# Performance work log

Hardware: AMD Instinct MI355X
Metric: run time of the kernel (lower is better)

Reference implementation:

```python
import jax, jax.numpy as jnp
import numpy as np
import math

FEAT, HID, EMB, NCLS = 128, 128, 64, 10
N, E = 50000, 1600000
RATIO = 0.8


def graph_conv(x, src, dst, valid, w_rel, b_rel, w_root):
    # PyG GraphConv: out = lin_rel(sum_{j->i} x_j) + lin_root(x_i)
    msg = jnp.where(valid[:, None], x[src], 0.0)  # [E, C]
    seg = jnp.where(valid, dst, x.shape[0])       # invalid -> dummy bucket
    agg = jax.ops.segment_sum(msg, seg, num_segments=x.shape[0] + 1)[:-1]
    return agg @ w_rel.T + b_rel + x @ w_root.T


def topk_pool(x, src, dst, valid, weight):
    # PyG TopKPooling: score = tanh((x . w) / ||w||); keep top ceil(ratio*N)
    score = jnp.tanh((x @ weight) / jnp.linalg.norm(weight))
    k = int(math.ceil(RATIO * x.shape[0]))
    _, perm = jax.lax.top_k(score, k)
    xp = x[perm] * score[perm][:, None]
    mapping = jnp.full((x.shape[0],), -1, dtype=src.dtype)
    mapping = mapping.at[perm].set(jnp.arange(k, dtype=src.dtype))
    nsrc, ndst = mapping[src], mapping[dst]
    nvalid = valid & (nsrc >= 0) & (ndst >= 0)
    return xp, nsrc, ndst, nvalid, perm


def setup_inputs() -> dict:
    key = jax.random.key(0)
    ks = jax.random.split(key, 24)
    s = 0.05
    inp = {
        'x': jax.random.normal(ks[0], (N, FEAT), dtype=jnp.float32),
        'edge_index': jax.random.randint(ks[1], (2, E), 0, N, dtype=jnp.int32),
        'w1_rel': jax.random.normal(ks[2], (HID, FEAT)) * s,
        'w1_root': jax.random.normal(ks[3], (HID, FEAT)) * s,
        'b1': jnp.zeros((HID,), jnp.float32),
        'p1_w': jax.random.normal(ks[4], (HID,)) * s,
        'w2_rel': jax.random.normal(ks[5], (EMB, HID)) * s,
        'w2_root': jax.random.normal(ks[6], (EMB, HID)) * s,
        'b2': jnp.zeros((EMB,), jnp.float32),
        'p2_w': jax.random.normal(ks[7], (EMB,)) * s,
        'w3_rel': jax.random.normal(ks[8], (EMB, EMB)) * s,
        'w3_root': jax.random.normal(ks[9], (EMB, EMB)) * s,
        'b3': jnp.zeros((EMB,), jnp.float32),
        'w4_rel': jax.random.normal(ks[10], (HID, EMB)) * s,
        'w4_root': jax.random.normal(ks[11], (HID, EMB)) * s,
        'b4': jnp.zeros((HID,), jnp.float32),
        'w5_rel': jax.random.normal(ks[12], (FEAT, HID)) * s,
        'w5_root': jax.random.normal(ks[13], (FEAT, HID)) * s,
        'b5': jnp.zeros((FEAT,), jnp.float32),
        'lin_w': jax.random.normal(ks[14], (NCLS, FEAT)) * s,
        'lin_b': jnp.zeros((NCLS,), jnp.float32),
    }
    return inp


def reference(x, edge_index, w1_rel, w1_root, b1, p1_w, w2_rel, w2_root, b2, p2_w,
              w3_rel, w3_root, b3, w4_rel, w4_root, b4, w5_rel, w5_root, b5,
              lin_w, lin_b):
    src0, dst0 = edge_index[0], edge_index[1]
    valid0 = jnp.ones((src0.shape[0],), dtype=bool)

    x1 = jax.nn.relu(graph_conv(x, src0, dst0, valid0, w1_rel, b1, w1_root))
    xp1, src1, dst1, valid1, perm1 = topk_pool(x1, src0, dst0, valid0, p1_w)
    x2 = jax.nn.relu(graph_conv(xp1, src1, dst1, valid1, w2_rel, b2, w2_root))
    xp2, src2, dst2, valid2, perm2 = topk_pool(x2, src1, dst1, valid1, p2_w)
    x3 = jax.nn.relu(graph_conv(xp2, src2, dst2, valid2, w3_rel, b3, w3_root))
    # Unpool1: scatter x3 into zeros shaped like x2, then skip-add
    u1 = jnp.zeros((x2.shape[0], x3.shape[1]), x3.dtype).at[perm2].set(x3) + x2
    x4 = jax.nn.relu(graph_conv(u1, src1, dst1, valid1, w4_rel, b4, w4_root))
    # Unpool2
    u2 = jnp.zeros((x1.shape[0], x4.shape[1]), x4.dtype).at[perm1].set(x4) + x1
    x5 = jax.nn.relu(graph_conv(u2, src0, dst0, valid0, w5_rel, b5, w5_root))
    return jax.nn.log_softmax(x5 @ lin_w.T + lin_b, axis=-1)
```

## Files before the change

### kernel.cpp

```cpp
#include <hip/hip_runtime.h>
#include <hip/hip_bf16.h>
#include <math.h>

#define N0 50000
#define E0 1600000
#define K1 40000
#define K2 32000
#define FEAT 128
#define HID 128
#define EMB 64
#define NCLS 10

#define RADIX_BINS 4096

#define NB 391
#define PB_CH 8192
#define BCAP 5120

#define SCHUNK 2048

typedef __bf16 v8bf __attribute__((ext_vector_type(8)));
typedef __bf16 v4bf __attribute__((ext_vector_type(4)));
typedef float  v4f  __attribute__((ext_vector_type(4)));
typedef unsigned short u16;

static __device__ __forceinline__ unsigned f2key(float f) {
    unsigned u = __float_as_uint(f);
    return (u & 0x80000000u) ? ~u : (u | 0x80000000u);
}

__global__ void detect_dtype_kernel(const unsigned* __restrict__ w, int n, int* __restrict__ flag) {
    __shared__ int tot;
    if (threadIdx.x == 0) tot = 0;
    __syncthreads();
    int cnt = 0;
    for (int i = threadIdx.x; i < n; i += 256) {
        unsigned lo = w[i] & 0xFFFFu;
        unsigned e = (lo >> 7) & 0xFFu;
        cnt += (e >= 143);
    }
    atomicAdd(&tot, cnt);
    __syncthreads();
    if (threadIdx.x == 0) flag[0] = (tot > n / 8) ? 1 : 0;
}

static __device__ __forceinline__ float load_as_f32(const void* in, long long i, int isF32) {
    if (isF32) return ((const float*)in)[i];
    unsigned short h = ((const unsigned short*)in)[i];
    return __uint_as_float(((unsigned)h) << 16);
}

__global__ void x_convert_kernel(const void* __restrict__ in, float* __restrict__ xf,
                                 __bf16* __restrict__ hi, __bf16* __restrict__ lo, int n,
                                 const int* __restrict__ flag) {
    int i = blockIdx.x * 256 + threadIdx.x;
    if (i >= n) return;
    float v = load_as_f32(in, i, *flag);
    __bf16 h = (__bf16)v;
    int row = i >> 7, c = i & 127;
    xf[(((size_t)(c >> 4)) * N0 + row) * 16 + (c & 15)] = v;
    hi[i] = h; lo[i] = (__bf16)(v - (float)h);
}

struct SplitJob { const void* src; __bf16* hi; __bf16* lo; int n; };
struct SplitJobs { SplitJob j[10]; };
__global__ void split_all_kernel(SplitJobs jobs, const int* __restrict__ flag) {
    SplitJob jb = jobs.j[blockIdx.y];
    int i = blockIdx.x * 256 + threadIdx.x;
    if (i >= jb.n) return;
    float v = load_as_f32(jb.src, i, *flag);
    __bf16 h = (__bf16)v;
    jb.hi[i] = h; jb.lo[i] = (__bf16)(v - (float)h);
}

struct F32Job { const void* src; float* dst; int n; };
struct F32Jobs { F32Job j[9]; };
__global__ void f32_all_kernel(F32Jobs jobs, const int* __restrict__ flag) {
    F32Job jb = jobs.j[blockIdx.x];
    for (int i = threadIdx.x; i < jb.n; i += 256) jb.dst[i] = load_as_f32(jb.src, i, *flag);
}

__global__ void scan_reduce_kernel(const int* __restrict__ deg, int M, int* __restrict__ btot) {
    int t = threadIdx.x;
    int idx = blockIdx.x * SCHUNK + t * 8;
    int s = 0;
    if (idx + 8 <= M) {
        int4 a = *(const int4*)(deg + idx);
        int4 b = *(const int4*)(deg + idx + 4);
        s = a.x + a.y + a.z + a.w + b.x + b.y + b.z + b.w;
    } else {
        for (int k = 0; k < 8; ++k) if (idx + k < M) s += deg[idx + k];
    }
    for (int off = 32; off >= 1; off >>= 1) s += __shfl_xor(s, off, 64);
    __shared__ int ws[4];
    if ((t & 63) == 0) ws[t >> 6] = s;
    __syncthreads();
    if (t == 0) btot[blockIdx.x] = ws[0] + ws[1] + ws[2] + ws[3];
}

__global__ void scan_offsets_kernel(const int* __restrict__ btot, int nb,
                                    int* __restrict__ boff, int* __restrict__ totPtr) {
    int t = threadIdx.x;
    int v = (t < nb) ? btot[t] : 0;
    int incl = v;
    for (int off = 1; off < 64; off <<= 1) {
        int u = __shfl_up(incl, off, 64);
        if (t >= off) incl += u;
    }
    if (t < nb) boff[t] = incl - v;
    if (t == 63 && totPtr) totPtr[0] = incl;
}

__global__ void scan_apply_kernel(const int* __restrict__ deg, int M, const int* __restrict__ boff,
                                  int* __restrict__ rowptr) {
    int t = threadIdx.x;
    int lane = t & 63, wave = t >> 6;
    int idx = blockIdx.x * SCHUNK + t * 8;
    int v[8];
#pragma unroll
    for (int k = 0; k < 8; ++k) v[k] = (idx + k < M) ? deg[idx + k] : 0;
    int s = 0;
#pragma unroll
    for (int k = 0; k < 8; ++k) { int tmp = v[k]; v[k] = s; s += tmp; }
    int incl = s;
    for (int off = 1; off < 64; off <<= 1) {
        int u = __shfl_up(incl, off, 64);
        if (lane >= off) incl += u;
    }
    int texcl = incl - s;
    __shared__ int ws[4];
    if (lane == 63) ws[wave] = incl;
    __syncthreads();
    int woff = 0;
    for (int w = 0; w < 4; ++w) if (w < wave) woff += ws[w];
    int off0 = boff[blockIdx.x] + woff + texcl;
#pragma unroll
    for (int k = 0; k < 8; ++k) {
        int j = idx + k;
        if (j < M) rowptr[j] = off0 + v[k];
    }
}

struct SelCtl { unsigned long long prefix; int kRem; int counter; };

__global__ void scan_reduce_keys_kernel(const unsigned long long* __restrict__ keys, int M,
                                        const SelCtl* __restrict__ ctl, int* __restrict__ btot) {
    unsigned long long thr = ctl->prefix;
    int t = threadIdx.x;
    int idx = blockIdx.x * SCHUNK + t * 8;
    int s = 0;
#pragma unroll
    for (int k = 0; k < 8; ++k) if (idx + k < M) s += (keys[idx + k] >= thr);
    for (int off = 32; off >= 1; off >>= 1) s += __shfl_xor(s, off, 64);
    __shared__ int ws[4];
    if ((t & 63) == 0) ws[t >> 6] = s;
    __syncthreads();
    if (t == 0) btot[blockIdx.x] = ws[0] + ws[1] + ws[2] + ws[3];
}

__global__ void scan_apply_keys_kernel(const unsigned long long* __restrict__ keys, int M,
                                       const SelCtl* __restrict__ ctl, const int* __restrict__ boff,
                                       int* __restrict__ pos) {
    unsigned long long thr = ctl->prefix;
    int t = threadIdx.x;
    int lane = t & 63, wave = t >> 6;
    int idx = blockIdx.x * SCHUNK + t * 8;
    int v[8];
#pragma unroll
    for (int k = 0; k < 8; ++k) v[k] = (idx + k < M) ? (int)(keys[idx + k] >= thr) : 0;
    int s = 0;
#pragma unroll
    for (int k = 0; k < 8; ++k) { int tmp = v[k]; v[k] = s; s += tmp; }
    int incl = s;
    for (int off = 1; off < 64; off <<= 1) {
        int u = __shfl_up(incl, off, 64);
        if (lane >= off) incl += u;
    }
    int texcl = incl - s;
    __shared__ int ws[4];
    if (lane == 63) ws[wave] = incl;
    __syncthreads();
    int woff = 0;
    for (int w = 0; w < 4; ++w) if (w < wave) woff += ws[w];
    int off0 = boff[blockIdx.x] + woff + texcl;
#pragma unroll
    for (int k = 0; k < 8; ++k) {
        int j = idx + k;
        if (j < M) pos[j] = off0 + v[k];
    }
}

__global__ void bucket_count_kernel(const int* __restrict__ dst, int E, int* __restrict__ bktCnt) {
    __shared__ int cnt[NB];
    for (int b = threadIdx.x; b < NB; b += 256) cnt[b] = 0;
    __syncthreads();
    int e = blockIdx.x * PB_CH;
    int e1 = E < e + PB_CH ? E : e + PB_CH;
    for (int i = e + threadIdx.x; i < e1; i += 256)
        atomicAdd(&cnt[dst[i] >> 7], 1);
    __syncthreads();
    for (int b = threadIdx.x; b < NB; b += 256) {
        int c = cnt[b];
        if (c) atomicAdd(&bktCnt[b], c);
    }
}

__global__ void scan_nb_kernel(const int* __restrict__ bktCnt, int* __restrict__ bktBase,
                               int* __restrict__ bcur, int* __restrict__ rpM, int E) {
    __shared__ int sc[512];
    int t = threadIdx.x;
    int v = (t < NB) ? bktCnt[t] : 0;
    sc[t] = v;
    __syncthreads();
    for (int off = 1; off < 512; off <<= 1) {
        int u = 0;
        if (t >= off) u = sc[t - off];
        __syncthreads();
        if (t >= off) sc[t] += u;
        __syncthreads();
    }
    if (t < NB) {
        int base = sc[t] - v;
        bktBase[t] = base;
        bcur[t] = base;
    }
    if (t == 0) { bktBase[NB] = E; rpM[0] = E; }
}

__global__ void edge_partition_kernel(const int* __restrict__ src, const int* __restrict__ dst, int E,
                                      int* __restrict__ bcur, unsigned* __restrict__ pairBuf) {
    __shared__ int cnt[NB];
    __shared__ int bas[NB];
    for (int b = threadIdx.x; b < NB; b += 256) cnt[b] = 0;
    __syncthreads();
    int e0 = blockIdx.x * PB_CH;
    int e1 = E < e0 + PB_CH ? E : e0 + PB_CH;
    for (int e = e0 + threadIdx.x; e < e1; e += 256)
        atomicAdd(&cnt[dst[e] >> 7], 1);
    __syncthreads();
    for (int b = threadIdx.x; b < NB; b += 256) {
        int c = cnt[b];
        bas[b] = c ? atomicAdd(&bcur[b], c) : 0;
        cnt[b] = 0;
    }
    __syncthreads();
    for (int e = e0 + threadIdx.x; e < e1; e += 256) {
        int s = src[e];
        int d = dst[e];
        int b = d >> 7;
        int r = atomicAdd(&cnt[b], 1);
        unsigned pv = ((unsigned)(d & 127) << 16) | (unsigned)s;
        __builtin_nontemporal_store(pv, pairBuf + bas[b] + r);
    }
}

__global__ void bucket_fill_kernel(const unsigned* __restrict__ pairBuf, const int* __restrict__ bktBase,
                                   int Mrows, u16* __restrict__ cols, int* __restrict__ rowptr) {
    int b = blockIdx.x;
    int d0 = b << 7;
    int d1 = d0 + 128; if (d1 > Mrows) d1 = Mrows;
    int segBase = bktBase[b], segEnd = bktBase[b + 1];
    int size = segEnd - segBase;
    int tid = threadIdx.x;
    __shared__ int cnt[128];
    __shared__ int sc[128];
    __shared__ int cur[128];
    __shared__ u16 stage[BCAP];
    if (tid < 128) cnt[tid] = 0;
    __syncthreads();
    for (int t = tid; t < size; t += 256)
        atomicAdd(&cnt[pairBuf[segBase + t] >> 16], 1);
    __syncthreads();
    if (tid < 128) sc[tid] = cnt[tid];
    __syncthreads();
    for (int off = 1; off < 128; off <<= 1) {
        int u = 0;
        if (tid < 128 && tid >= off) u = sc[tid - off];
        __syncthreads();
        if (tid < 128 && tid >= off) sc[tid] += u;
        __syncthreads();
    }
    if (tid < 128) {
        int excl = sc[tid] - cnt[tid];
        cur[tid] = excl;
        if (d0 + tid < d1) rowptr[d0 + tid] = segBase + excl;
    }
    __syncthreads();
    if (size <= BCAP) {
        for (int t = tid; t < size; t += 256) {
            unsigned p = pairBuf[segBase + t];
            int pos = atomicAdd(&cur[p >> 16], 1);
            stage[pos] = (u16)(p & 0xFFFFu);
        }
        __syncthreads();
        for (int t = tid; t < size; t += 256)
            __builtin_nontemporal_store(stage[t], cols + segBase + t);
    } else {
        for (int t = tid; t < size; t += 256) {
            unsigned p = pairBuf[segBase + t];
            int pos = atomicAdd(&cur[p >> 16], 1);
            cols[segBase + pos] = (u16)(p & 0xFFFFu);
        }
    }
}

__global__ void deg_filter_kernel(const int* __restrict__ rowptr, const u16* __restrict__ cols,
                                  const int* __restrict__ map, int Mold, int* __restrict__ deg) {
    int d = blockIdx.x * 256 + threadIdx.x;
    if (d >= Mold) return;
    int nd = map[d];
    if (nd < 0) return;
    int b = rowptr[d], e = rowptr[d + 1];
    int c = 0;
    for (int j = b; j < e; ++j) c += (map[cols[j]] >= 0);
    deg[nd] = c;
}

__global__ void csr_filter_fill_kernel(const int* __restrict__ rowptr, const u16* __restrict__ cols,
                                       const int* __restrict__ map, int Mold,
                                       const int* __restrict__ newrp, u16* __restrict__ ncols) {
    int d = blockIdx.x * 256 + threadIdx.x;
    if (d >= Mold) return;
    int nd = map[d];
    if (nd < 0) return;
    int w = newrp[nd];
    int b = rowptr[d], e = rowptr[d + 1];
    for (int j = b; j < e; ++j) {
        int ns = map[cols[j]];
        if (ns >= 0) ncols[w++] = (u16)ns;
    }
}

template<int C>
__global__ void __launch_bounds__(256, 8)
aggregate_kernel(const int* __restrict__ rowptr, const u16* __restrict__ cols,
                 const float* __restrict__ xs, __bf16* __restrict__ aggHi,
                 __bf16* __restrict__ aggLo, int M) {
    const int SW = C / 8;
    const int LPR = SW / 4;
    const int RPB = 256 / LPR;
    int sl = blockIdx.x & 7;
    int n  = (blockIdx.x >> 3) * RPB + threadIdx.x / LPR;
    int c4 = threadIdx.x % LPR;
    if (n >= M) return;
    const float* xsl = xs + (size_t)sl * M * SW + (size_t)c4 * 4;
    int b = rowptr[n], e = rowptr[n + 1];
    float4 s = {0.f, 0.f, 0.f, 0.f};
    int j = b;
    for (; j + 8 <= e; j += 8) {
        int i0 = cols[j],     i1 = cols[j + 1], i2 = cols[j + 2], i3 = cols[j + 3];
        int i4 = cols[j + 4], i5 = cols[j + 5], i6 = cols[j + 6], i7 = cols[j + 7];
        float4 v0 = *(const float4*)(xsl + (size_t)i0 * SW);
        float4 v1 = *(const float4*)(xsl + (size_t)i1 * SW);
        float4 v2 = *(const float4*)(xsl + (size_t)i2 * SW);
        float4 v3 = *(const float4*)(xsl + (size_t)i3 * SW);
        float4 v4 = *(const float4*)(xsl + (size_t)i4 * SW);
        float4 v5 = *(const float4*)(xsl + (size_t)i5 * SW);
        float4 v6 = *(const float4*)(xsl + (size_t)i6 * SW);
        float4 v7 = *(const float4*)(xsl + (size_t)i7 * SW);
        s.x += v0.x; s.y += v0.y; s.z += v0.z; s.w += v0.w;
        s.x += v1.x; s.y += v1.y; s.z += v1.z; s.w += v1.w;
        s.x += v2.x; s.y += v2.y; s.z += v2.z; s.w += v2.w;
        s.x += v3.x; s.y += v3.y; s.z += v3.z; s.w += v3.w;
        s.x += v4.x; s.y += v4.y; s.z += v4.z; s.w += v4.w;
        s.x += v5.x; s.y += v5.y; s.z += v5.z; s.w += v5.w;
        s.x += v6.x; s.y += v6.y; s.z += v6.z; s.w += v6.w;
        s.x += v7.x; s.y += v7.y; s.z += v7.z; s.w += v7.w;
    }
    for (; j < e; ++j) {
        int i0 = cols[j];
        float4 v0 = *(const float4*)(xsl + (size_t)i0 * SW);
        s.x += v0.x; s.y += v0.y; s.z += v0.z; s.w += v0.w;
    }
    v4bf h, l;
    h[0] = (__bf16)s.x; l[0] = (__bf16)(s.x - (float)h[0]);
    h[1] = (__bf16)s.y; l[1] = (__bf16)(s.y - (float)h[1]);
    h[2] = (__bf16)s.z; l[2] = (__bf16)(s.z - (float)h[2]);
    h[3] = (__bf16)s.w; l[3] = (__bf16)(s.w - (float)h[3]);
    size_t o = ((size_t)sl * M + n) * SW + c4 * 4;
    __builtin_nontemporal_store(h, (v4bf*)(aggHi + o));
    __builtin_nontemporal_store(l, (v4bf*)(aggLo + o));
}

template<int Cin, int Cout>
__global__ void linear_mfma_kernel(int M,
                                   const __bf16* __restrict__ Ahi, const __bf16* __restrict__ Alo,
                                   const __bf16* __restrict__ WaHi, const __bf16* __restrict__ WaLo,
                                   const __bf16* __restrict__ Bhi, const __bf16* __restrict__ Blo,
                                   const __bf16* __restrict__ WbHi, const __bf16* __restrict__ WbLo,
                                   const float* __restrict__ bias, float* __restrict__ outF) {
    constexpr int NG = Cout / 16;
    constexpr int SW = Cin / 8;
    int wave = threadIdx.x >> 6;
    int lane = threadIdx.x & 63;
    int m = lane & 15, quad = lane >> 4;
    int row0 = blockIdx.x * 64 + wave * 16;
    int ra = row0 + m; if (ra > M - 1) ra = M - 1;

    v4f acc[NG];
#pragma unroll
    for (int g = 0; g < NG; ++g) acc[g] = (v4f){0.f, 0.f, 0.f, 0.f};

#pragma unroll
    for (int ks = 0; ks < Cin / 32; ++ks) {
        int col0 = ks * 32 + quad * 8;
        int sl = col0 / SW, off = col0 % SW;
        size_t aoff = ((size_t)sl * M + ra) * SW + off;
        v8bf ah = *(const v8bf*)(Ahi + aoff);
        v8bf al = *(const v8bf*)(Alo + aoff);
#pragma unroll
        for (int g = 0; g < NG; ++g) {
            size_t woff = (size_t)(g * 16 + m) * Cin + ks * 32 + quad * 8;
            v8bf bh = *(const v8bf*)(WaHi + woff);
            v8bf bl = *(const v8bf*)(WaLo + woff);
            acc[g] = __builtin_amdgcn_mfma_f32_16x16x32_bf16(ah, bh, acc[g], 0, 0, 0);
            acc[g] = __builtin_amdgcn_mfma_f32_16x16x32_bf16(ah, bl, acc[g], 0, 0, 0);
            acc[g] = __builtin_amdgcn_mfma_f32_16x16x32_bf16(al, bh, acc[g], 0, 0, 0);
        }
    }
#pragma unroll
    for (int ks = 0; ks < Cin / 32; ++ks) {
        size_t aoff = (size_t)ra * Cin + ks * 32 + quad * 8;
        v8bf ah = *(const v8bf*)(Bhi + aoff);
        v8bf al = *(const v8bf*)(Blo + aoff);
#pragma unroll
        for (int g = 0; g < NG; ++g) {
            size_t woff = (size_t)(g * 16 + m) * Cin + ks * 32 + quad * 8;
            v8bf bh = *(const v8bf*)(WbHi + woff);
            v8bf bl = *(const v8bf*)(WbLo + woff);
            acc[g] = __builtin_amdgcn_mfma_f32_16x16x32_bf16(ah, bh, acc[g], 0, 0, 0);
            acc[g] = __builtin_amdgcn_mfma_f32_16x16x32_bf16(ah, bl, acc[g], 0, 0, 0);
            acc[g] = __builtin_amdgcn_mfma_f32_16x16x32_bf16(al, bh, acc[g], 0, 0, 0);
        }
    }

#pragma unroll
    for (int g = 0; g < NG; ++g) {
        int col = g * 16 + m;
        float bv = bias[col];
#pragma unroll
        for (int r = 0; r < 4; ++r) {
            int row = row0 + quad * 4 + r;
            if (row < M) outF[(size_t)row * Cout + col] = fmaxf(acc[g][r] + bv, 0.f);
        }
    }
}

template<int C>
__global__ void score_kernel(const float* __restrict__ xin, const float* __restrict__ w,
                             int M, float* __restrict__ score, unsigned long long* __restrict__ keys) {
    int row = blockIdx.x * 4 + (threadIdx.x >> 6);
    int lane = threadIdx.x & 63;
    if (row >= M) return;
    float p = 0.f, q = 0.f;
#pragma unroll
    for (int c = lane; c < C; c += 64) {
        float wc = w[c];
        float xc = xin[(size_t)row * C + c];
        p += xc * wc; q += wc * wc;
    }
#pragma unroll
    for (int off = 32; off >= 1; off >>= 1) {
        p += __shfl_xor(p, off, 64);
        q += __shfl_xor(q, off, 64);
    }
    if (lane == 0) {
        float arg = p / sqrtf(q);
        float sc = (float)tanh((double)arg);
        score[row] = sc;
        keys[row] = ((unsigned long long)f2key(sc) << 16) |
                    (unsigned long long)(0xFFFFu ^ (unsigned)row);
    }
}

__global__ void radix_hist_kernel(const unsigned long long* __restrict__ keys, int N,
                                  int* __restrict__ hist, const SelCtl* __restrict__ ctl, int pass) {
    __shared__ int lh[RADIX_BINS];
    for (int b = threadIdx.x; b < RADIX_BINS; b += 256) lh[b] = 0;
    __syncthreads();
    int shift = 36 - 12 * pass;
    unsigned long long pref = (pass > 0) ? ctl->prefix : 0ull;
    for (int i = blockIdx.x * 256 + threadIdx.x; i < N; i += gridDim.x * 256) {
        unsigned long long key = keys[i];
        if (pass > 0 && (key >> (shift + 12)) != pref) continue;
        atomicAdd(&lh[(int)((key >> shift) & 0xFFFull)], 1);
    }
    __syncthreads();
    for (int b = threadIdx.x; b < RADIX_BINS; b += 256) {
        int c = lh[b];
        if (c) atomicAdd(&hist[b], c);
    }
}

__global__ void radix_select_kernel(int* __restrict__ hist, SelCtl* __restrict__ ctl,
                                    int K, int pass) {
    __shared__ int wtot[16];
    int t = threadIdx.x;
    int lane = t & 63, wave = t >> 6;
    int kRem = (pass == 0) ? K : ctl->kRem;
    unsigned long long oldPrefix = (pass == 0) ? 0ull : ctl->prefix;
    int base = t * 4;
    int h0 = hist[base], h1 = hist[base + 1], h2 = hist[base + 2], h3 = hist[base + 3];
    int tot = h0 + h1 + h2 + h3;
    int incl = tot;
#pragma unroll
    for (int off = 1; off < 64; off <<= 1) {
        int u = __shfl_down(incl, off, 64);
        if (lane + off < 64) incl += u;
    }
    if (lane == 0) wtot[wave] = incl;
    __syncthreads();
    int wsuf = 0;
#pragma unroll
    for (int w = 0; w < 16; ++w) if (w > wave) wsuf += wtot[w];
    int sExcl = wsuf + (incl - tot);
    if (sExcl < kRem && kRem <= sExcl + tot) {
        int c = sExcl;
        int hv[4] = {h0, h1, h2, h3};
        for (int k = 3; k >= 0; --k) {
            int h = hv[k];
            if (c + h >= kRem) {
                ctl->prefix = (oldPrefix << 12) | (unsigned long long)(base + k);
                ctl->kRem = kRem - c;
                ctl->counter = 0;
                break;
            }
            c += h;
        }
    }
    hist[base] = 0; hist[base + 1] = 0; hist[base + 2] = 0; hist[base + 3] = 0;
}

__global__ void finalize_map_keys_kernel(const unsigned long long* __restrict__ keys,
                                         const int* __restrict__ pos, int N,
                                         const SelCtl* __restrict__ ctl,
                                         int* __restrict__ perm, int* __restrict__ mapping) {
    int i = blockIdx.x * 256 + threadIdx.x;
    if (i >= N) return;
    if (keys[i] >= ctl->prefix) { int r = pos[i]; perm[r] = i; mapping[i] = r; }
    else mapping[i] = -1;
}

template<int C>
__global__ void pool_apply_kernel(const float* __restrict__ xin, const float* __restrict__ score,
                                  const int* __restrict__ perm, float* __restrict__ xpF,
                                  __bf16* __restrict__ xpHi, __bf16* __restrict__ xpLo, int K) {
    const int CH = C / 4;
    const int SW = C / 8;
    int tid = blockIdx.x * 256 + threadIdx.x;
    int j = tid / CH, c4 = tid % CH;
    if (j >= K) return;
    int src = perm[j];
    float s = score[src];
    float4 v = ((const float4*)(xin + (size_t)src * C))[c4];
    v.x *= s; v.y *= s; v.z *= s; v.w *= s;
    int sl = (c4 * 4) / SW, off = (c4 * 4) % SW;
    *(float4*)(xpF + ((size_t)sl * K + j) * SW + off) = v;
    v4bf h, l;
    h[0] = (__bf16)v.x; l[0] = (__bf16)(v.x - (float)h[0]);
    h[1] = (__bf16)v.y; l[1] = (__bf16)(v.y - (float)h[1]);
    h[2] = (__bf16)v.z; l[2] = (__bf16)(v.z - (float)h[2]);
    h[3] = (__bf16)v.w; l[3] = (__bf16)(v.w - (float)h[3]);
    *(v4bf*)(xpHi + (size_t)j * C + c4 * 4) = h;
    *(v4bf*)(xpLo + (size_t)j * C + c4 * 4) = l;
}

template<int C>
__global__ void unpool_add_kernel(const float* __restrict__ base, const float* __restrict__ deep,
                                  const int* __restrict__ mapping, float* __restrict__ uF,
                                  __bf16* __restrict__ uHi, __bf16* __restrict__ uLo, int M) {
    const int CH = C / 4;
    const int SW = C / 8;
    int tid = blockIdx.x * 256 + threadIdx.x;
    int j = tid / CH, c4 = tid % CH;
    if (j >= M) return;
    float4 v = ((const float4*)(base + (size_t)j * C))[c4];
    int m = mapping[j];
    if (m >= 0) {
        float4 d = ((const float4*)(deep + (size_t)m * C))[c4];
        v.x += d.x; v.y += d.y; v.z += d.z; v.w += d.w;
    }
    int sl = (c4 * 4) / SW, off = (c4 * 4) % SW;
    *(float4*)(uF + ((size_t)sl * M + j) * SW + off) = v;
    v4bf h, l;
    h[0] = (__bf16)v.x; l[0] = (__bf16)(v.x - (float)h[0]);
    h[1] = (__bf16)v.y; l[1] = (__bf16)(v.y - (float)h[1]);
    h[2] = (__bf16)v.z; l[2] = (__bf16)(v.z - (float)h[2]);
    h[3] = (__bf16)v.w; l[3] = (__bf16)(v.w - (float)h[3]);
    *(v4bf*)(uHi + (size_t)j * C + c4 * 4) = h;
    *(v4bf*)(uLo + (size_t)j * C + c4 * 4) = l;
}

__global__ void head_kernel(const float* __restrict__ x5, const float* __restrict__ lw,
                            const float* __restrict__ lb, void* __restrict__ out, int M,
                            const int* __restrict__ flag) {
    int row = blockIdx.x * 4 + (threadIdx.x >> 6);
    int lane = threadIdx.x & 63;
    if (row >= M) return;
    float a0 = x5[(size_t)row * 128 + lane];
    float a1 = x5[(size_t)row * 128 + 64 + lane];
    float d[NCLS];
#pragma unroll
    for (int o = 0; o < NCLS; ++o) {
        float p = a0 * lw[o * 128 + lane] + a1 * lw[o * 128 + 64 + lane];
#pragma unroll
        for (int off = 32; off >= 1; off >>= 1) p += __shfl_xor(p, off, 64);
        d[o] = p + lb[o];
    }
    float mx = d[0];
#pragma unroll
    for (int o = 1; o < NCLS; ++o) mx = fmaxf(mx, d[o]);
    float s = 0.f;
#pragma unroll
    for (int o = 0; o < NCLS; ++o) s += expf(d[o] - mx);
    float lse = mx + logf(s);
    if (lane < NCLS) {
        float v = d[0];
#pragma unroll
        for (int o = 1; o < NCLS; ++o) if (lane == o) v = d[o];
        float r = v - lse;
        if (*flag) ((float*)out)[(size_t)row * NCLS + lane] = r;
        else ((__hip_bfloat16*)out)[(size_t)row * NCLS + lane] = __float2bfloat16(r);
    }
}

extern "C" void kernel_launch(void* const* d_in, const int* in_sizes, int n_in,
                              void* d_out, int out_size, void* d_ws, size_t ws_size,
                              hipStream_t stream) {
    const void* x_raw   = d_in[0];
    const int*  ei      = (const int*)d_in[1];
    const void* w1_rel  = d_in[2];
    const void* w1_root = d_in[3];
    const void* b1      = d_in[4];
    const void* p1w     = d_in[5];
    const void* w2_rel  = d_in[6];
    const void* w2_root = d_in[7];
    const void* b2      = d_in[8];
    const void* p2w     = d_in[9];
    const void* w3_rel  = d_in[10];
    const void* w3_root = d_in[11];
    const void* b3      = d_in[12];
    const void* w4_rel  = d_in[13];
    const void* w4_root = d_in[14];
    const void* b4      = d_in[15];
    const void* w5_rel  = d_in[16];
    const void* w5_root = d_in[17];
    const void* b5      = d_in[18];
    const void* lw      = d_in[19];
    const void* lb      = d_in[20];

    char* base = (char*)d_ws;
    size_t off = 0;
    auto alloc = [&](size_t bytes) -> void* {
        void* p = base + off;
        off = (off + bytes + 255) & ~(size_t)255;
        return p;
    };
    int* flag = (int*)alloc(256);
    __bf16* w1rHi = (__bf16*)alloc(HID * FEAT * 2); __bf16* w1rLo = (__bf16*)alloc(HID * FEAT * 2);
    __bf16* w1tHi = (__bf16*)alloc(HID * FEAT * 2); __bf16* w1tLo = (__bf16*)alloc(HID * FEAT * 2);
    __bf16* w2rHi = (__bf16*)alloc(EMB * HID * 2);  __bf16* w2rLo = (__bf16*)alloc(EMB * HID * 2);
    __bf16* w2tHi = (__bf16*)alloc(EMB * HID * 2);  __bf16* w2tLo = (__bf16*)alloc(EMB * HID * 2);
    __bf16* w3rHi = (__bf16*)alloc(EMB * EMB * 2);  __bf16* w3rLo = (__bf16*)alloc(EMB * EMB * 2);
    __bf16* w3tHi = (__bf16*)alloc(EMB * EMB * 2);  __bf16* w3tLo = (__bf16*)alloc(EMB * EMB * 2);
    __bf16* w4rHi = (__bf16*)alloc(HID * EMB * 2);  __bf16* w4rLo = (__bf16*)alloc(HID * EMB * 2);
    __bf16* w4tHi = (__bf16*)alloc(HID * EMB * 2);  __bf16* w4tLo = (__bf16*)alloc(HID * EMB * 2);
    __bf16* w5rHi = (__bf16*)alloc(FEAT * HID * 2); __bf16* w5rLo = (__bf16*)alloc(FEAT * HID * 2);
    __bf16* w5tHi = (__bf16*)alloc(FEAT * HID * 2); __bf16* w5tLo = (__bf16*)alloc(FEAT * HID * 2);
    float* b1f = (float*)alloc(HID * 4);
    float* b2f = (float*)alloc(EMB * 4);
    float* b3f = (float*)alloc(EMB * 4);
    float* b4f = (float*)alloc(HID * 4);
    float* b5f = (float*)alloc(FEAT * 4);
    float* p1f = (float*)alloc(HID * 4);
    float* p2f = (float*)alloc(EMB * 4);
    float* lwf = (float*)alloc(NCLS * FEAT * 4);
    float* lbf = (float*)alloc(NCLS * 4);
    float* score = (float*)alloc((size_t)N0 * 4);
    unsigned long long* keys = (unsigned long long*)alloc((size_t)N0 * 8);
    int* hist = (int*)alloc((size_t)RADIX_BINS * 4);
    SelCtl* ctl = (SelCtl*)alloc(256);
    int* btot = (int*)alloc(64 * 4);
    int* boff = (int*)alloc(64 * 4);
    int* perm1 = (int*)alloc((size_t)K1 * 4);
    int* map1  = (int*)alloc((size_t)N0 * 4);
    int* perm2 = (int*)alloc((size_t)K2 * 4);
    int* map2  = (int*)alloc((size_t)K1 * 4);
    int* pos   = (int*)alloc((size_t)(N0 + 1) * 4);
    int* deg   = (int*)alloc((size_t)(N0 + 1) * 4);
    int* rp0   = (int*)alloc((size_t)(N0 + 1) * 4);
    int* rp1   = (int*)alloc((size_t)(K1 + 1) * 4);
    int* rp2   = (int*)alloc((size_t)(K2 + 1) * 4);
    int* bktCnt = (int*)alloc((size_t)(NB + 1) * 4);
    int* bktBase= (int*)alloc((size_t)(NB + 1) * 4);
    int* bcur  = (int*)alloc((size_t)NB * 4);
    u16* cols0 = (u16*)alloc((size_t)E0 * 2);
    u16* cols1 = (u16*)alloc((size_t)E0 * 2);
    u16* cols2 = (u16*)alloc((size_t)E0 * 2);
    char* ubuf = (char*)alloc((size_t)K1 * 64 * 4 + (size_t)N0 * 128 * 4);
    unsigned* pairBuf = (unsigned*)ubuf;
    float* u1s = (float*)ubuf;
    float* u2s = (float*)(ubuf + (size_t)K1 * 64 * 4);
    char*   arenaX  = (char*)alloc((size_t)N0 * 128 * 4);
    __bf16* arenaHi = (__bf16*)alloc((size_t)N0 * 128 * 2);
    __bf16* arenaLo = (__bf16*)alloc((size_t)N0 * 128 * 2);
    __bf16* aggHi   = (__bf16*)alloc((size_t)N0 * 128 * 2);
    __bf16* aggLo   = (__bf16*)alloc((size_t)N0 * 128 * 2);
    float*  x1f     = (float*)alloc((size_t)N0 * 128 * 4);
    float*  x2f     = (float*)alloc((size_t)K1 * 64 * 4);

    float* xf   = (float*)arenaX;
    float* xp1f = (float*)arenaX;
    float* xp2f = (float*)arenaX;
    float* x3f  = (float*)(arenaX + 8388608);
    float* x4f  = (float*)arenaX;
    float* x5f  = (float*)arenaX;
    __bf16 *xHi = arenaHi,  *xLo = arenaLo;
    __bf16 *xp1Hi = arenaHi, *xp1Lo = arenaLo;
    __bf16 *xp2Hi = arenaHi, *xp2Lo = arenaLo;
    __bf16 *u1Hi = arenaHi,  *u1Lo = arenaLo;
    __bf16 *u2Hi = arenaHi,  *u2Lo = arenaLo;

    const int* src0 = ei;
    const int* dst0 = ei + E0;

    auto g = [](long long n, int b) -> unsigned { return (unsigned)((n + b - 1) / b); };

    auto run_scan = [&](const int* degp, int M, int* rowp) {
        int nb = (M + SCHUNK - 1) / SCHUNK;
        scan_reduce_kernel<<<nb, 256, 0, stream>>>(degp, M, btot);
        scan_offsets_kernel<<<1, 64, 0, stream>>>(btot, nb, boff, rowp + M);
        scan_apply_kernel<<<nb, 256, 0, stream>>>(degp, M, boff, rowp);
    };
    auto run_scan_keys = [&](const unsigned long long* keysP, int M, int* posArr) {
        int nb = (M + SCHUNK - 1) / SCHUNK;
        scan_reduce_keys_kernel<<<nb, 256, 0, stream>>>(keysP, M, ctl, btot);
        scan_offsets_kernel<<<1, 64, 0, stream>>>(btot, nb, boff, posArr + M);
        scan_apply_keys_kernel<<<nb, 256, 0, stream>>>(keysP, M, ctl, boff, posArr);
    };

    detect_dtype_kernel<<<1, 256, 0, stream>>>((const unsigned*)x_raw, 4096, flag);
    hipMemsetAsync(hist, 0, (size_t)RADIX_BINS * 4, stream);
    hipMemsetAsync(bktCnt, 0, (size_t)(NB + 1) * 4, stream);
    x_convert_kernel<<<g((long long)N0 * FEAT, 256), 256, 0, stream>>>(x_raw, xf, xHi, xLo, N0 * FEAT, flag);
    {
        SplitJobs sj;
        sj.j[0] = {w1_rel,  w1rHi, w1rLo, HID * FEAT};
        sj.j[1] = {w1_root, w1tHi, w1tLo, HID * FEAT};
        sj.j[2] = {w2_rel,  w2rHi, w2rLo, EMB * HID};
        sj.j[3] = {w2_root, w2tHi, w2tLo, EMB * HID};
        sj.j[4] = {w3_rel,  w3rHi, w3rLo, EMB * EMB};
        sj.j[5] = {w3_root, w3tHi, w3tLo, EMB * EMB};
        sj.j[6] = {w4_rel,  w4rHi, w4rLo, HID * EMB};
        sj.j[7] = {w4_root, w4tHi, w4tLo, HID * EMB};
        sj.j[8] = {w5_rel,  w5rHi, w5rLo, FEAT * HID};
        sj.j[9] = {w5_root, w5tHi, w5tLo, FEAT * HID};
        dim3 grid(g(HID * FEAT, 256), 10);
        split_all_kernel<<<grid, 256, 0, stream>>>(sj, flag);
    }
    {
        F32Jobs fj;
        fj.j[0] = {b1, b1f, HID};
        fj.j[1] = {b2, b2f, EMB};
        fj.j[2] = {b3, b3f, EMB};
        fj.j[3] = {b4, b4f, HID};
        fj.j[4] = {b5, b5f, FEAT};
        fj.j[5] = {p1w, p1f, HID};
        fj.j[6] = {p2w, p2f, EMB};
        fj.j[7] = {lw, lwf, NCLS * FEAT};
        fj.j[8] = {lb, lbf, NCLS};
        f32_all_kernel<<<9, 256, 0, stream>>>(fj, flag);
    }

    bucket_count_kernel<<<g(E0, PB_CH), 256, 0, stream>>>(dst0, E0, bktCnt);
    scan_nb_kernel<<<1, 512, 0, stream>>>(bktCnt, bktBase, bcur, rp0 + N0, E0);
    edge_partition_kernel<<<g(E0, PB_CH), 256, 0, stream>>>(src0, dst0, E0, bcur, pairBuf);
    bucket_fill_kernel<<<NB, 256, 0, stream>>>(pairBuf, bktBase, N0, cols0, rp0);

    aggregate_kernel<128><<<g(N0, 64) * 8, 256, 0, stream>>>(rp0, cols0, xf, aggHi, aggLo, N0);
    linear_mfma_kernel<128, 128><<<g(N0, 64), 256, 0, stream>>>(N0, aggHi, aggLo, w1rHi, w1rLo,
                                                                xHi, xLo, w1tHi, w1tLo, b1f, x1f);

    score_kernel<128><<<g(N0, 4), 256, 0, stream>>>(x1f, p1f, N0, score, keys);
    for (int pass = 0; pass < 4; ++pass) {
        radix_hist_kernel<<<64, 256, 0, stream>>>(keys, N0, hist, ctl, pass);
        radix_select_kernel<<<1, 1024, 0, stream>>>(hist, ctl, K1, pass);
    }
    run_scan_keys(keys, N0, pos);
    finalize_map_keys_kernel<<<g(N0, 256), 256, 0, stream>>>(keys, pos, N0, ctl, perm1, map1);
    pool_apply_kernel<128><<<g((long long)K1 * 32, 256), 256, 0, stream>>>(x1f, score, perm1, xp1f, xp1Hi, xp1Lo, K1);

    deg_filter_kernel<<<g(N0, 256), 256, 0, stream>>>(rp0, cols0, map1, N0, deg);
    run_scan(deg, K1, rp1);
    csr_filter_fill_kernel<<<g(N0, 256), 256, 0, stream>>>(rp0, cols0, map1, N0, rp1, cols1);

    aggregate_kernel<128><<<g(K1, 64) * 8, 256, 0, stream>>>(rp1, cols1, xp1f, aggHi, aggLo, K1);
    linear_mfma_kernel<128, 64><<<g(K1, 64), 256, 0, stream>>>(K1, aggHi, aggLo, w2rHi, w2rLo,
                                                               xp1Hi, xp1Lo, w2tHi, w2tLo, b2f, x2f);

    score_kernel<64><<<g(K1, 4), 256, 0, stream>>>(x2f, p2f, K1, score, keys);
    for (int pass = 0; pass < 4; ++pass) {
        radix_hist_kernel<<<64, 256, 0, stream>>>(keys, K1, hist, ctl, pass);
        radix_select_kernel<<<1, 1024, 0, stream>>>(hist, ctl, K2, pass);
    }
    run_scan_keys(keys, K1, pos);
    finalize_map_keys_kernel<<<g(K1, 256), 256, 0, stream>>>(keys, pos, K1, ctl, perm2, map2);
    pool_apply_kernel<64><<<g((long long)K2 * 16, 256), 256, 0, stream>>>(x2f, score, perm2, xp2f, xp2Hi, xp2Lo, K2);

    deg_filter_kernel<<<g(K1, 256), 256, 0, stream>>>(rp1, cols1, map2, K1, deg);
    run_scan(deg, K2, rp2);
    csr_filter_fill_kernel<<<g(K1, 256), 256, 0, stream>>>(rp1, cols1, map2, K1, rp2, cols2);

    aggregate_kernel<64><<<g(K2, 128) * 8, 256, 0, stream>>>(rp2, cols2, xp2f, aggHi, aggLo, K2);
    linear_mfma_kernel<64, 64><<<g(K2, 64), 256, 0, stream>>>(K2, aggHi, aggLo, w3rHi, w3rLo,
                                                              xp2Hi, xp2Lo, w3tHi, w3tLo, b3f, x3f);

    unpool_add_kernel<64><<<g((long long)K1 * 16, 256), 256, 0, stream>>>(x2f, x3f, map2, u1s, u1Hi, u1Lo, K1);

    aggregate_kernel<64><<<g(K1, 128) * 8, 256, 0, stream>>>(rp1, cols1, u1s, aggHi, aggLo, K1);
    linear_mfma_kernel<64, 128><<<g(K1, 64), 256, 0, stream>>>(K1, aggHi, aggLo, w4rHi, w4rLo,
                                                               u1Hi, u1Lo, w4tHi, w4tLo, b4f, x4f);

    unpool_add_kernel<128><<<g((long long)N0 * 32, 256), 256, 0, stream>>>(x1f, x4f, map1, u2s, u2Hi, u2Lo, N0);

    aggregate_kernel<128><<<g(N0, 64) * 8, 256, 0, stream>>>(rp0, cols0, u2s, aggHi, aggLo, N0);
    linear_mfma_kernel<128, 128><<<g(N0, 64), 256, 0, stream>>>(N0, aggHi, aggLo, w5rHi, w5rLo,
                                                                u2Hi, u2Lo, w5tHi, w5tLo, b5f, x5f);

    head_kernel<<<g(N0, 4), 256, 0, stream>>>(x5f, lwf, lbf, d_out, N0, flag);
}
```

Before: 939.7 us.

## Fuse TopK scoring into linear epilogue and use single-pass lookback scan

```diff
diff --git a/kernel.cpp b/kernel.cpp
--- a/kernel.cpp
+++ b/kernel.cpp
@@ -28,6 +28,8 @@
     unsigned u = __float_as_uint(f);
     return (u & 0x80000000u) ? ~u : (u | 0x80000000u);
 }
+
+struct SelCtl { unsigned long long prefix; int kRem; int counter; };
 
 __global__ void detect_dtype_kernel(const unsigned* __restrict__ w, int n, int* __restrict__ flag) {
     __shared__ int tot;
@@ -80,45 +82,26 @@
     for (int i = threadIdx.x; i < jb.n; i += 256) jb.dst[i] = load_as_f32(jb.src, i, *flag);
 }
 
-__global__ void scan_reduce_kernel(const int* __restrict__ deg, int M, int* __restrict__ btot) {
-    int t = threadIdx.x;
-    int idx = blockIdx.x * SCHUNK + t * 8;
-    int s = 0;
-    if (idx + 8 <= M) {
-        int4 a = *(const int4*)(deg + idx);
-        int4 b = *(const int4*)(deg + idx + 4);
-        s = a.x + a.y + a.z + a.w + b.x + b.y + b.z + b.w;
-    } else {
-        for (int k = 0; k < 8; ++k) if (idx + k < M) s += deg[idx + k];
-    }
-    for (int off = 32; off >= 1; off >>= 1) s += __shfl_xor(s, off, 64);
-    __shared__ int ws[4];
-    if ((t & 63) == 0) ws[t >> 6] = s;
-    __syncthreads();
-    if (t == 0) btot[blockIdx.x] = ws[0] + ws[1] + ws[2] + ws[3];
-}
-
-__global__ void scan_offsets_kernel(const int* __restrict__ btot, int nb,
-                                    int* __restrict__ boff, int* __restrict__ totPtr) {
-    int t = threadIdx.x;
-    int v = (t < nb) ? btot[t] : 0;
-    int incl = v;
-    for (int off = 1; off < 64; off <<= 1) {
-        int u = __shfl_up(incl, off, 64);
-        if (t >= off) incl += u;
-    }
-    if (t < nb) boff[t] = incl - v;
-    if (t == 63 && totPtr) totPtr[0] = incl;
-}
-
-__global__ void scan_apply_kernel(const int* __restrict__ deg, int M, const int* __restrict__ boff,
-                                  int* __restrict__ rowptr) {
+template<int KEYS>
+__global__ void lookback_scan_kernel(const int* __restrict__ deg,
+                                     const unsigned long long* __restrict__ keys,
+                                     const SelCtl* __restrict__ ctl, int M,
+                                     int* __restrict__ flags,
+                                     int* __restrict__ rowp,
+                                     int* __restrict__ perm,
+                                     int* __restrict__ mapping) {
+    int b = blockIdx.x;
     int t = threadIdx.x;
     int lane = t & 63, wave = t >> 6;
-    int idx = blockIdx.x * SCHUNK + t * 8;
+    int idx = b * SCHUNK + t * 8;
+    unsigned long long thr = KEYS ? ctl->prefix : 0ull;
     int v[8];
 #pragma unroll
-    for (int k = 0; k < 8; ++k) v[k] = (idx + k < M) ? deg[idx + k] : 0;
+    for (int k = 0; k < 8; ++k) {
+        int j = idx + k;
+        if (KEYS) v[k] = (j < M) ? (int)(keys[j] >= thr) : 0;
+        else      v[k] = (j < M) ? deg[j] : 0;
+    }
     int s = 0;
 #pragma unroll
     for (int k = 0; k < 8; ++k) { int tmp = v[k]; v[k] = s; s += tmp; }
@@ -129,64 +112,40 @@
     }
     int texcl = incl - s;
     __shared__ int ws[4];
+    __shared__ int pfxs;
     if (lane == 63) ws[wave] = incl;
     __syncthreads();
-    int woff = 0;
-    for (int w = 0; w < 4; ++w) if (w < wave) woff += ws[w];
-    int off0 = boff[blockIdx.x] + woff + texcl;
-#pragma unroll
-    for (int k = 0; k < 8; ++k) {
-        int j = idx + k;
-        if (j < M) rowptr[j] = off0 + v[k];
-    }
-}
-
-struct SelCtl { unsigned long long prefix; int kRem; int counter; };
-
-__global__ void scan_reduce_keys_kernel(const unsigned long long* __restrict__ keys, int M,
-                                        const SelCtl* __restrict__ ctl, int* __restrict__ btot) {
-    unsigned long long thr = ctl->prefix;
-    int t = threadIdx.x;
-    int idx = blockIdx.x * SCHUNK + t * 8;
-    int s = 0;
-#pragma unroll
-    for (int k = 0; k < 8; ++k) if (idx + k < M) s += (keys[idx + k] >= thr);
-    for (int off = 32; off >= 1; off >>= 1) s += __shfl_xor(s, off, 64);
-    __shared__ int ws[4];
-    if ((t & 63) == 0) ws[t >> 6] = s;
-    __syncthreads();
-    if (t == 0) btot[blockIdx.x] = ws[0] + ws[1] + ws[2] + ws[3];
-}
-
-__global__ void scan_apply_keys_kernel(const unsigned long long* __restrict__ keys, int M,
-                                       const SelCtl* __restrict__ ctl, const int* __restrict__ boff,
-                                       int* __restrict__ pos) {
-    unsigned long long thr = ctl->prefix;
-    int t = threadIdx.x;
-    int lane = t & 63, wave = t >> 6;
-    int idx = blockIdx.x * SCHUNK + t * 8;
-    int v[8];
-#pragma unroll
-    for (int k = 0; k < 8; ++k) v[k] = (idx + k < M) ? (int)(keys[idx + k] >= thr) : 0;
-    int s = 0;
-#pragma unroll
-    for (int k = 0; k < 8; ++k) { int tmp = v[k]; v[k] = s; s += tmp; }
-    int incl = s;
-    for (int off = 1; off < 64; off <<= 1) {
-        int u = __shfl_up(incl, off, 64);
-        if (lane >= off) incl += u;
-    }
-    int texcl = incl - s;
-    __shared__ int ws[4];
-    if (lane == 63) ws[wave] = incl;
-    __syncthreads();
-    int woff = 0;
-    for (int w = 0; w < 4; ++w) if (w < wave) woff += ws[w];
-    int off0 = boff[blockIdx.x] + woff + texcl;
-#pragma unroll
-    for (int k = 0; k < 8; ++k) {
-        int j = idx + k;
-        if (j < M) pos[j] = off0 + v[k];
+    int woff = 0, T = 0;
+    for (int w = 0; w < 4; ++w) { if (w < wave) woff += ws[w]; T += ws[w]; }
+    if (t == 0) {
+        __threadfence();
+        atomicExch(&flags[b], T + 1);
+        int sum = 0;
+        for (int p = 0; p < b; ++p) {
+            int f;
+            while ((f = atomicAdd(&flags[p], 0)) == 0) { }
+            sum += f - 1;
+        }
+        pfxs = sum;
+    }
+    __syncthreads();
+    int off0 = pfxs + woff + texcl;
+    if (!KEYS) {
+#pragma unroll
+        for (int k = 0; k < 8; ++k) {
+            int j = idx + k;
+            if (j < M) rowp[j] = off0 + v[k];
+        }
+        if (b == gridDim.x - 1 && t == 255) rowp[M] = pfxs + T;
+    } else {
+#pragma unroll
+        for (int k = 0; k < 8; ++k) {
+            int j = idx + k;
+            if (j < M) {
+                if (keys[j] >= thr) { int r = off0 + v[k]; perm[r] = j; mapping[j] = r; }
+                else mapping[j] = -1;
+            }
+        }
     }
 }
 
@@ -382,15 +341,17 @@
     __builtin_nontemporal_store(l, (v4bf*)(aggLo + o));
 }
 
-template<int Cin, int Cout>
+template<int Cin, int Cout, bool SCORE>
 __global__ void linear_mfma_kernel(int M,
                                    const __bf16* __restrict__ Ahi, const __bf16* __restrict__ Alo,
                                    const __bf16* __restrict__ WaHi, const __bf16* __restrict__ WaLo,
                                    const __bf16* __restrict__ Bhi, const __bf16* __restrict__ Blo,
                                    const __bf16* __restrict__ WbHi, const __bf16* __restrict__ WbLo,
-                                   const float* __restrict__ bias, float* __restrict__ outF) {
+                                   const float* __restrict__ bias, float* __restrict__ outF,
+                                   const float* __restrict__ sw, float* __restrict__ score,
+                                   unsigned long long* __restrict__ keys) {
     constexpr int NG = Cout / 16;
-    constexpr int SW = Cin / 8;
+    constexpr int SW2 = Cin / 8;
     int wave = threadIdx.x >> 6;
     int lane = threadIdx.x & 63;
     int m = lane & 15, quad = lane >> 4;
@@ -404,8 +365,8 @@
 #pragma unroll
     for (int ks = 0; ks < Cin / 32; ++ks) {
         int col0 = ks * 32 + quad * 8;
-        int sl = col0 / SW, off = col0 % SW;
-        size_t aoff = ((size_t)sl * M + ra) * SW + off;
+        int sl = col0 / SW2, off = col0 % SW2;
+        size_t aoff = ((size_t)sl * M + ra) * SW2 + off;
         v8bf ah = *(const v8bf*)(Ahi + aoff);
         v8bf al = *(const v8bf*)(Alo + aoff);
 #pragma unroll
@@ -444,32 +405,40 @@
             if (row < M) outF[(size_t)row * Cout + col] = fmaxf(acc[g][r] + bv, 0.f);
         }
     }
-}
-
-template<int C>
-__global__ void score_kernel(const float* __restrict__ xin, const float* __restrict__ w,
-                             int M, float* __restrict__ score, unsigned long long* __restrict__ keys) {
-    int row = blockIdx.x * 4 + (threadIdx.x >> 6);
-    int lane = threadIdx.x & 63;
-    if (row >= M) return;
-    float p = 0.f, q = 0.f;
-#pragma unroll
-    for (int c = lane; c < C; c += 64) {
-        float wc = w[c];
-        float xc = xin[(size_t)row * C + c];
-        p += xc * wc; q += wc * wc;
-    }
-#pragma unroll
-    for (int off = 32; off >= 1; off >>= 1) {
-        p += __shfl_xor(p, off, 64);
-        q += __shfl_xor(q, off, 64);
-    }
-    if (lane == 0) {
-        float arg = p / sqrtf(q);
-        float sc = (float)tanh((double)arg);
-        score[row] = sc;
-        keys[row] = ((unsigned long long)f2key(sc) << 16) |
-                    (unsigned long long)(0xFFFFu ^ (unsigned)row);
+
+    if (SCORE) {
+        float wv[NG];
+        float q = 0.f;
+#pragma unroll
+        for (int g = 0; g < NG; ++g) { wv[g] = sw[g * 16 + m]; q += wv[g] * wv[g]; }
+#pragma unroll
+        for (int off = 1; off < 16; off <<= 1) q += __shfl_xor(q, off, 64);
+        float pr[4];
+#pragma unroll
+        for (int r = 0; r < 4; ++r) {
+            float p = 0.f;
+#pragma unroll
+            for (int g = 0; g < NG; ++g) {
+                float ov = fmaxf(acc[g][r] + bias[g * 16 + m], 0.f);
+                p += ov * wv[g];
+            }
+#pragma unroll
+            for (int off = 1; off < 16; off <<= 1) p += __shfl_xor(p, off, 64);
+            pr[r] = p;
+        }
+        if (m == 0) {
+            float rq = sqrtf(q);
+#pragma unroll
+            for (int r = 0; r < 4; ++r) {
+                int row = row0 + quad * 4 + r;
+                if (row < M) {
+                    float sc = (float)tanh((double)(pr[r] / rq));
+                    score[row] = sc;
+                    keys[row] = ((unsigned long long)f2key(sc) << 16) |
+                                (unsigned long long)(0xFFFFu ^ (unsigned)row);
+                }
+            }
+        }
     }
 }
 
@@ -529,16 +498,6 @@
         }
     }
     hist[base] = 0; hist[base + 1] = 0; hist[base + 2] = 0; hist[base + 3] = 0;
-}
-
-__global__ void finalize_map_keys_kernel(const unsigned long long* __restrict__ keys,
-                                         const int* __restrict__ pos, int N,
-                                         const SelCtl* __restrict__ ctl,
-                                         int* __restrict__ perm, int* __restrict__ mapping) {
-    int i = blockIdx.x * 256 + threadIdx.x;
-    if (i >= N) return;
-    if (keys[i] >= ctl->prefix) { int r = pos[i]; perm[r] = i; mapping[i] = r; }
-    else mapping[i] = -1;
 }
 
 template<int C>
@@ -678,20 +637,22 @@
     float* lbf = (float*)alloc(NCLS * 4);
     float* score = (float*)alloc((size_t)N0 * 4);
     unsigned long long* keys = (unsigned long long*)alloc((size_t)N0 * 8);
-    int* hist = (int*)alloc((size_t)RADIX_BINS * 4);
+    char* zeroArena = (char*)alloc(RADIX_BINS * 4 + 2048 + 1024);
+    int* hist    = (int*)zeroArena;
+    int* bktCnt  = (int*)(zeroArena + RADIX_BINS * 4);
+    int* flags0  = (int*)(zeroArena + RADIX_BINS * 4 + 2048);
+    int* flags1  = flags0 + 64;
+    int* flags2  = flags0 + 128;
+    int* flags3  = flags0 + 192;
     SelCtl* ctl = (SelCtl*)alloc(256);
-    int* btot = (int*)alloc(64 * 4);
-    int* boff = (int*)alloc(64 * 4);
     int* perm1 = (int*)alloc((size_t)K1 * 4);
     int* map1  = (int*)alloc((size_t)N0 * 4);
     int* perm2 = (int*)alloc((size_t)K2 * 4);
     int* map2  = (int*)alloc((size_t)K1 * 4);
-    int* pos   = (int*)alloc((size_t)(N0 + 1) * 4);
     int* deg   = (int*)alloc((size_t)(N0 + 1) * 4);
     int* rp0   = (int*)alloc((size_t)(N0 + 1) * 4);
     int* rp1   = (int*)alloc((size_t)(K1 + 1) * 4);
     int* rp2   = (int*)alloc((size_t)(K2 + 1) * 4);
-    int* bktCnt = (int*)alloc((size_t)(NB + 1) * 4);
     int* bktBase= (int*)alloc((size_t)(NB + 1) * 4);
     int* bcur  = (int*)alloc((size_t)NB * 4);
     u16* cols0 = (u16*)alloc((size_t)E0 * 2);
@@ -726,22 +687,8 @@
 
     auto g = [](long long n, int b) -> unsigned { return (unsigned)((n + b - 1) / b); };
 
-    auto run_scan = [&](const int* degp, int M, int* rowp) {
-        int nb = (M + SCHUNK - 1) / SCHUNK;
-        scan_reduce_kernel<<<nb, 256, 0, stream>>>(degp, M, btot);
-        scan_offsets_kernel<<<1, 64, 0, stream>>>(btot, nb, boff, rowp + M);
-        scan_apply_kernel<<<nb, 256, 0, stream>>>(degp, M, boff, rowp);
-    };
-    auto run_scan_keys = [&](const unsigned long long* keysP, int M, int* posArr) {
-        int nb = (M + SCHUNK - 1) / SCHUNK;
-        scan_reduce_keys_kernel<<<nb, 256, 0, stream>>>(keysP, M, ctl, btot);
-        scan_offsets_kernel<<<1, 64, 0, stream>>>(btot, nb, boff, posArr + M);
-        scan_apply_keys_kernel<<<nb, 256, 0, stream>>>(keysP, M, ctl, boff, posArr);
-    };
-
     detect_dtype_kernel<<<1, 256, 0, stream>>>((const unsigned*)x_raw, 4096, flag);
-    hipMemsetAsync(hist, 0, (size_t)RADIX_BINS * 4, stream);
-    hipMemsetAsync(bktCnt, 0, (size_t)(NB + 1) * 4, stream);
+    hipMemsetAsync(zeroArena, 0, RADIX_BINS * 4 + 2048 + 1024, stream);
     x_convert_kernel<<<g((long long)N0 * FEAT, 256), 256, 0, stream>>>(x_raw, xf, xHi, xLo, N0 * FEAT, flag);
     {
         SplitJobs sj;
@@ -778,54 +725,59 @@
     bucket_fill_kernel<<<NB, 256, 0, stream>>>(pairBuf, bktBase, N0, cols0, rp0);
 
     aggregate_kernel<128><<<g(N0, 64) * 8, 256, 0, stream>>>(rp0, cols0, xf, aggHi, aggLo, N0);
-    linear_mfma_kernel<128, 128><<<g(N0, 64), 256, 0, stream>>>(N0, aggHi, aggLo, w1rHi, w1rLo,
-                                                                xHi, xLo, w1tHi, w1tLo, b1f, x1f);
-
-    score_kernel<128><<<g(N0, 4), 256, 0, stream>>>(x1f, p1f, N0, score, keys);
+    linear_mfma_kernel<128, 128, true><<<g(N0, 64), 256, 0, stream>>>(N0, aggHi, aggLo, w1rHi, w1rLo,
+                                                                      xHi, xLo, w1tHi, w1tLo, b1f, x1f,
+                                                                      p1f, score, keys);
+
     for (int pass = 0; pass < 4; ++pass) {
         radix_hist_kernel<<<64, 256, 0, stream>>>(keys, N0, hist, ctl, pass);
         radix_select_kernel<<<1, 1024, 0, stream>>>(hist, ctl, K1, pass);
     }
-    run_scan_keys(keys, N0, pos);
-    finalize_map_keys_kernel<<<g(N0, 256), 256, 0, stream>>>(keys, pos, N0, ctl, perm1, map1);
+    lookback_scan_kernel<1><<<g(N0, SCHUNK), 256, 0, stream>>>(nullptr, keys, ctl, N0, flags0,
+                                                               nullptr, perm1, map1);
     pool_apply_kernel<128><<<g((long long)K1 * 32, 256), 256, 0, stream>>>(x1f, score, perm1, xp1f, xp1Hi, xp1Lo, K1);
 
     deg_filter_kernel<<<g(N0, 256), 256, 0, stream>>>(rp0, cols0, map1, N0, deg);
-    run_scan(deg, K1, rp1);
+    lookback_scan_kernel<0><<<g(K1, SCHUNK), 256, 0, stream>>>(deg, nullptr, nullptr, K1, flags1,
+                                                               rp1, nullptr, nullptr);
     csr_filter_fill_kernel<<<g(N0, 256), 256, 0, stream>>>(rp0, cols0, map1, N0, rp1, cols1);
 
     aggregate_kernel<128><<<g(K1, 64) * 8, 256, 0, stream>>>(rp1, cols1, xp1f, aggHi, aggLo, K1);
-    linear_mfma_kernel<128, 64><<<g(K1, 64), 256, 0, stream>>>(K1, aggHi, aggLo, w2rHi, w2rLo,
-                                                               xp1Hi, xp1Lo, w2tHi, w2tLo, b2f, x2f);
-
-    score_kernel<64><<<g(K1, 4), 256, 0, stream>>>(x2f, p2f, K1, score, keys);
+    linear_mfma_kernel<128, 64, true><<<g(K1, 64), 256, 0, stream>>>(K1, aggHi, aggLo, w2rHi, w2rLo,
+                                                                     xp1Hi, xp1Lo, w2tHi, w2tLo, b2f, x2f,
+                                                                     p2f, score, keys);
+
     for (int pass = 0; pass < 4; ++pass) {
         radix_hist_kernel<<<64, 256, 0, stream>>>(keys, K1, hist, ctl, pass);
         radix_select_kernel<<<1, 1024, 0, stream>>>(hist, ctl, K2, pass);
     }
-    run_scan_keys(keys, K1, pos);
-    finalize_map_keys_kernel<<<g(K1, 256), 256, 0, stream>>>(keys, pos, K1, ctl, perm2, map2);
+    lookback_scan_kernel<1><<<g(K1, SCHUNK), 256, 0, stream>>>(nullptr, keys, ctl, K1, flags2,
+                                                               nullptr, perm2, map2);
     pool_apply_kernel<64><<<g((long long)K2 * 16, 256), 256, 0, stream>>>(x2f, score, perm2, xp2f, xp2Hi, xp2Lo, K2);
 
     deg_filter_kernel<<<g(K1, 256), 256, 0, stream>>>(rp1, cols1, map2, K1, deg);
-    run_scan(deg, K2, rp2);
+    lookback_scan_kernel<0><<<g(K2, SCHUNK), 256, 0, stream>>>(deg, nullptr, nullptr, K2, flags3,
+                                                               rp2, nullptr, nullptr);
     csr_filter_fill_kernel<<<g(K1, 256), 256, 0, stream>>>(rp1, cols1, map2, K1, rp2, cols2);
 
     aggregate_kernel<64><<<g(K2, 128) * 8, 256, 0, stream>>>(rp2, cols2, xp2f, aggHi, aggLo, K2);
-    linear_mfma_kernel<64, 64><<<g(K2, 64), 256, 0, stream>>>(K2, aggHi, aggLo, w3rHi, w3rLo,
-                                                              xp2Hi, xp2Lo, w3tHi, w3tLo, b3f, x3f);
+    linear_mfma_kernel<64, 64, false><<<g(K2, 64), 256, 0, stream>>>(K2, aggHi, aggLo, w3rHi, w3rLo,
+                                                                     xp2Hi, xp2Lo, w3tHi, w3tLo, b3f, x3f,
+                                                                     nullptr, nullptr, nullptr);
 
     unpool_add_kernel<64><<<g((long long)K1 * 16, 256), 256, 0, stream>>>(x2f, x3f, map2, u1s, u1Hi, u1Lo, K1);
 
     aggregate_kernel<64><<<g(K1, 128) * 8, 256, 0, stream>>>(rp1, cols1, u1s, aggHi, aggLo, K1);
-    linear_mfma_kernel<64, 128><<<g(K1, 64), 256, 0, stream>>>(K1, aggHi, aggLo, w4rHi, w4rLo,
-                                                               u1Hi, u1Lo, w4tHi, w4tLo, b4f, x4f);
+    linear_mfma_kernel<64, 128, false><<<g(K1, 64), 256, 0, stream>>>(K1, aggHi, aggLo, w4rHi, w4rLo,
+                                                                      u1Hi, u1Lo, w4tHi, w4tLo, b4f, x4f,
+                                                                      nullptr, nullptr, nullptr);
 
     unpool_add_kernel<128><<<g((long long)N0 * 32, 256), 256, 0, stream>>>(x1f, x4f, map1, u2s, u2Hi, u2Lo, N0);
 
     aggregate_kernel<128><<<g(N0, 64) * 8, 256, 0, stream>>>(rp0, cols0, u2s, aggHi, aggLo, N0);
-    linear_mfma_kernel<128, 128><<<g(N0, 64), 256, 0, stream>>>(N0, aggHi, aggLo, w5rHi, w5rLo,
-                                                                u2Hi, u2Lo, w5tHi, w5tLo, b5f, x5f);
+    linear_mfma_kernel<128, 128, false><<<g(N0, 64), 256, 0, stream>>>(N0, aggHi, aggLo, w5rHi, w5rLo,
+                                                                       u2Hi, u2Lo, w5tHi, w5tLo, b5f, x5f,
+                                                                       nullptr, nullptr, nullptr);
 
     head_kernel<<<g(N0, 4), 256, 0, stream>>>(x5f, lwf, lbf, d_out, N0, flag);
 }
```

Result: faster. 911.1 us (-3.0%).
